# Kernel tuning notes

Hardware: AMD Instinct MI355X
Metric: run time of the kernel (lower is better)

The kernel has to match this reference:

```python
import jax, jax.numpy as jnp
import numpy as np

B, T, IDIM, ODIM, HDIM, CDIM = 8, 8192, 256, 256, 1024, 128


def setup_inputs() -> dict:
    key = jax.random.key(0)
    ks = jax.random.split(key, 7)
    s_enc = 1.0 / np.sqrt(IDIM)
    s_dec = 1.0 / np.sqrt(HDIM)
    return {
        "x": jax.random.normal(ks[0], (B, T, IDIM), jnp.float32),
        "mask_prev": jnp.zeros((B, T, HDIM), jnp.float32),
        "W_enc": jax.random.uniform(ks[1], (IDIM, HDIM), jnp.float32, -s_enc, s_enc),
        "b_enc": jax.random.uniform(ks[2], (HDIM,), jnp.float32, -s_enc, s_enc),
        "W_dec_self": jax.random.uniform(ks[3], (HDIM, IDIM), jnp.float32, -s_dec, s_dec),
        "b_dec_self": jax.random.uniform(ks[4], (IDIM,), jnp.float32, -s_dec, s_dec),
        "W_dec_src": jax.random.uniform(ks[5], (HDIM, ODIM), jnp.float32, -s_dec, s_dec),
        "b_dec_src": jax.random.uniform(ks[6], (ODIM,), jnp.float32, -s_dec, s_dec),
        "decoder_type": 0,  # 0 = 'self', 1 = 'src'
    }


def _topk_masks(h, cdim):
    # energy_pooling_mask with share=True: topk(k=2*cdim) of h^2 along hdim.
    energy = h * h  # [B,T,H]
    _, idx = jax.lax.top_k(energy, 2 * cdim)  # [B,T,2C] indices into H
    bi = jnp.arange(h.shape[0])[:, None, None]
    ti = jnp.arange(h.shape[1])[None, :, None]
    # scatter instead of materializing one_hot [B,T,2C,H]
    mask = jnp.zeros_like(h).at[bi, ti, idx[..., :cdim]].add(1.0)
    mask_share = jnp.zeros_like(h).at[bi, ti, idx].add(1.0)
    return mask, mask_share


def reference(x, mask_prev, W_enc, b_enc, W_dec_self, b_dec_self, W_dec_src, b_dec_src, decoder_type):
    # encoder
    h = jnp.einsum("bti,ih->bth", x, W_enc) + b_enc  # [B,T,H]
    # hidden_exclude_activation (mask_prev provided): zero previously-used units
    h = jnp.where(mask_prev > 0, 0.0, h)
    mask_cur, mask_cur_share = _topk_masks(h, CDIM)
    mask_new = mask_prev + mask_cur
    h = jnp.where(mask_cur_share > 0, h, 0.0)
    # decoder (idim == odim asserted in original)
    if decoder_type == 0:
        out = jnp.einsum("bth,ho->bto", h, W_dec_self) + b_dec_self
    else:
        out = jnp.einsum("bth,ho->bto", h, W_dec_src) + b_dec_src
    return out, mask_new
```

## Files before the change

kernel.cpp:

```cpp
#include <hip/hip_runtime.h>
#include <hip/hip_bf16.h>

#define B_ 8
#define T_ 8192
#define M_ (B_ * T_)
#define IDIM 256
#define HDIM 1024
#define ODIM 256
#define CDIM 128
#define OUT_OFF ((size_t)M_ * ODIM)

typedef __attribute__((ext_vector_type(4))) float floatx4;
typedef __attribute__((ext_vector_type(8))) short shortx8;

__global__ __launch_bounds__(256) void k0_convw(const float* __restrict__ Wself,
                                                const float* __restrict__ Wsrc,
                                                const int* __restrict__ dtype,
                                                __hip_bfloat16* __restrict__ WdT) {
    int id = blockIdx.x * 256 + threadIdx.x;
    int n = id >> 10;
    int k = id & 1023;
    const float* W = (*dtype == 0) ? Wself : Wsrc;
    WdT[id] = __float2bfloat16(W[(size_t)k * ODIM + n]);
}

__global__ __launch_bounds__(256) void k1_enc(const float* __restrict__ X,
                                              const float* __restrict__ W,
                                              const float* __restrict__ bias,
                                              float* __restrict__ H) {
    __shared__ __align__(16) float As[32][132];
    __shared__ __align__(16) float Bs[32][128];
    const int t  = threadIdx.x;
    const int m0 = blockIdx.x * 128;
    const int n0 = blockIdx.y * 128;
    const int tx = t & 15;
    const int ty = t >> 4;

    float acc[8][8];
#pragma unroll
    for (int i = 0; i < 8; ++i)
#pragma unroll
        for (int j = 0; j < 8; ++j) acc[i][j] = 0.0f;

    for (int kk = 0; kk < IDIM; kk += 32) {
#pragma unroll
        for (int r = 0; r < 4; ++r) {
            int idx = t + r * 256;
            int row = idx >> 3;
            int k4  = (idx & 7) << 2;
            float4 a = *(const float4*)(X + (size_t)(m0 + row) * IDIM + kk + k4);
            As[k4 + 0][row] = a.x;
            As[k4 + 1][row] = a.y;
            As[k4 + 2][row] = a.z;
            As[k4 + 3][row] = a.w;
        }
#pragma unroll
        for (int r = 0; r < 4; ++r) {
            int idx = t + r * 256;
            int row = idx >> 5;
            int c4  = (idx & 31) << 2;
            *(float4*)&Bs[row][c4] =
                *(const float4*)(W + (size_t)(kk + row) * HDIM + n0 + c4);
        }
        __syncthreads();

#pragma unroll 8
        for (int k = 0; k < 32; ++k) {
            float4 a0 = *(const float4*)&As[k][ty * 8];
            float4 a1 = *(const float4*)&As[k][ty * 8 + 4];
            float4 b0 = *(const float4*)&Bs[k][tx * 4];
            float4 b1 = *(const float4*)&Bs[k][tx * 4 + 64];
            float av[8] = {a0.x, a0.y, a0.z, a0.w, a1.x, a1.y, a1.z, a1.w};
            float bv[8] = {b0.x, b0.y, b0.z, b0.w, b1.x, b1.y, b1.z, b1.w};
#pragma unroll
            for (int i = 0; i < 8; ++i)
#pragma unroll
                for (int j = 0; j < 8; ++j)
                    acc[i][j] = fmaf(av[i], bv[j], acc[i][j]);
        }
        __syncthreads();
    }

#pragma unroll
    for (int i = 0; i < 8; ++i) {
        int gm = m0 + ty * 8 + i;
        float* o = H + (size_t)gm * HDIM + n0;
        float4 v0, v1;
        v0.x = acc[i][0] + bias[n0 + tx * 4 + 0];
        v0.y = acc[i][1] + bias[n0 + tx * 4 + 1];
        v0.z = acc[i][2] + bias[n0 + tx * 4 + 2];
        v0.w = acc[i][3] + bias[n0 + tx * 4 + 3];
        v1.x = acc[i][4] + bias[n0 + 64 + tx * 4 + 0];
        v1.y = acc[i][5] + bias[n0 + 64 + tx * 4 + 1];
        v1.z = acc[i][6] + bias[n0 + 64 + tx * 4 + 2];
        v1.w = acc[i][7] + bias[n0 + 64 + tx * 4 + 3];
        *(float4*)(o + tx * 4) = v0;
        *(float4*)(o + 64 + tx * 4) = v1;
    }
}

__device__ __forceinline__ unsigned int radix_kth(const unsigned int* u, int k,
                                                  unsigned int* hist,
                                                  unsigned int* res,
                                                  int lane, int* r_out) {
    unsigned int prefix = 0;
    int kk = k;
    for (int pass = 3; pass >= 0; --pass) {
        const int sh = pass * 8;
        hist[lane] = 0u; hist[lane + 64] = 0u;
        hist[lane + 128] = 0u; hist[lane + 192] = 0u;
        __syncthreads();
#pragma unroll
        for (int i = 0; i < 16; ++i) {
            bool matched = (pass == 3) || ((u[i] >> (sh + 8)) == (prefix >> (sh + 8)));
            if (matched) atomicAdd(&hist[(u[i] >> sh) & 0xFFu], 1u);
        }
        __syncthreads();
        unsigned int c0 = hist[lane * 4 + 0], c1 = hist[lane * 4 + 1];
        unsigned int c2 = hist[lane * 4 + 2], c3 = hist[lane * 4 + 3];
        unsigned int lt = c0 + c1 + c2 + c3;
        unsigned int s = lt;
#pragma unroll
        for (int off = 1; off < 64; off <<= 1) {
            unsigned int o = (unsigned int)__shfl_down((int)s, off, 64);
            if (lane + off < 64) s += o;
        }
        unsigned int gt_lanes = s - lt;
        unsigned int cs[4] = {c0, c1, c2, c3};
        unsigned int sf[4] = {c1 + c2 + c3, c2 + c3, c3, 0u};
#pragma unroll
        for (int q = 0; q < 4; ++q) {
            int gt = (int)(gt_lanes + sf[q]);
            int ge = gt + (int)cs[q];
            if (gt < kk && kk <= ge) {
                res[0] = (unsigned int)(lane * 4 + q);
                res[1] = (unsigned int)gt;
            }
        }
        __syncthreads();
        unsigned int b = res[0];
        kk -= (int)res[1];
        prefix |= (b << sh);
        __syncthreads();
    }
    *r_out = kk;
    return prefix;
}

__global__ __launch_bounds__(256) void k2_topk(const float* __restrict__ mask_prev,
                                               float* __restrict__ Hio,
                                               __hip_bfloat16* __restrict__ Abf) {
    __shared__ unsigned int hist[4][256];
    __shared__ unsigned int res[4][2];
    const int t = threadIdx.x;
    const int wave = t >> 6;
    const int lane = t & 63;
    const size_t row = (size_t)blockIdx.x * 4 + wave;
    const float* mp = mask_prev + row * HDIM;
    float* hrow = Hio + row * HDIM;

    float hv[16], mpv[16];
    unsigned int u[16];
#pragma unroll
    for (int i = 0; i < 16; ++i) {
        int j = lane + (i << 6);
        float m = mp[j];
        float h = hrow[j];
        h = (m > 0.0f) ? 0.0f : h;
        mpv[i] = m; hv[i] = h;
        float e = h * h;
        u[i] = __float_as_uint(e);
    }

    int r1, r2;
    unsigned int T1 = radix_kth(u, CDIM,     hist[wave], res[wave], lane, &r1);
    unsigned int T2 = radix_kth(u, 2 * CDIM, hist[wave], res[wave], lane, &r2);

    const unsigned long long below = (1ULL << lane) - 1ULL;
    int c1 = 0, c2 = 0;
#pragma unroll
    for (int i = 0; i < 16; ++i) {
        unsigned long long b1 = __ballot(u[i] == T1);
        unsigned long long b2 = __ballot(u[i] == T2);
        bool s1 = (u[i] > T1) || ((u[i] == T1) && (c1 + __popcll(b1 & below) < r1));
        bool s2 = (u[i] > T2) || ((u[i] == T2) && (c2 + __popcll(b2 & below) < r2));
        c1 += __popcll(b1);
        c2 += __popcll(b2);
        int j = lane + (i << 6);
        hrow[j] = mpv[i] + (s1 ? 1.0f : 0.0f);
        Abf[row * HDIM + j] = __float2bfloat16(s2 ? hv[i] : 0.0f);
    }
}

__global__ __launch_bounds__(256) void k3_dec(const __hip_bfloat16* __restrict__ A,
                                              const __hip_bfloat16* __restrict__ Bt,
                                              const float* __restrict__ bias_self,
                                              const float* __restrict__ bias_src,
                                              const int* __restrict__ dtype,
                                              float* __restrict__ Out) {
    __shared__ __align__(16) __hip_bfloat16 As[128 * 32];
    __shared__ __align__(16) __hip_bfloat16 Bs[128 * 32];
    const int t = threadIdx.x;
    const int lane = t & 63;
    const int wave = t >> 6;
    const int m0 = blockIdx.x * 128;
    const int n0 = blockIdx.y * 128;
    const int wr = wave >> 1;
    const int wc = wave & 1;
    const int quad = lane >> 4;
    const int rf = lane & 15;

    floatx4 acc[4][4];
    const floatx4 z = {0.0f, 0.0f, 0.0f, 0.0f};
#pragma unroll
    for (int i = 0; i < 4; ++i)
#pragma unroll
        for (int j = 0; j < 4; ++j) acc[i][j] = z;

    for (int kk = 0; kk < HDIM; kk += 32) {
#pragma unroll
        for (int p = 0; p < 2; ++p) {
            int l = p * 256 + t;
            int row = l >> 2;
            int kc = (l & 3) << 3;
            *(uint4*)&As[row * 32 + kc] =
                *(const uint4*)(A + (size_t)(m0 + row) * HDIM + kk + kc);
            *(uint4*)&Bs[row * 32 + kc] =
                *(const uint4*)(Bt + (size_t)(n0 + row) * HDIM + kk + kc);
        }
        __syncthreads();

        shortx8 af[4], bf[4];
#pragma unroll
        for (int i = 0; i < 4; ++i) {
            af[i] = *(const shortx8*)&As[(wr * 64 + i * 16 + rf) * 32 + quad * 8];
            bf[i] = *(const shortx8*)&Bs[(wc * 64 + i * 16 + rf) * 32 + quad * 8];
        }
#pragma unroll
        for (int mi = 0; mi < 4; ++mi)
#pragma unroll
            for (int nj = 0; nj < 4; ++nj)
                acc[mi][nj] = __builtin_amdgcn_mfma_f32_16x16x32_bf16(
                    af[mi], bf[nj], acc[mi][nj], 0, 0, 0);
        __syncthreads();
    }

    const float* bias = (*dtype == 0) ? bias_self : bias_src;
#pragma unroll
    for (int mi = 0; mi < 4; ++mi) {
#pragma unroll
        for (int nj = 0; nj < 4; ++nj) {
            int gn = n0 + wc * 64 + nj * 16 + rf;
            float bv = bias[gn];
            int gmb = m0 + wr * 64 + mi * 16 + quad * 4;
#pragma unroll
            for (int r2 = 0; r2 < 4; ++r2)
                Out[(size_t)(gmb + r2) * ODIM + gn] = acc[mi][nj][r2] + bv;
        }
    }
}

extern "C" void kernel_launch(void* const* d_in, const int* in_sizes, int n_in,
                              void* d_out, int out_size, void* d_ws, size_t ws_size,
                              hipStream_t stream) {
    const float* x          = (const float*)d_in[0];
    const float* mask_prev  = (const float*)d_in[1];
    const float* W_enc      = (const float*)d_in[2];
    const float* b_enc      = (const float*)d_in[3];
    const float* W_dec_self = (const float*)d_in[4];
    const float* b_dec_self = (const float*)d_in[5];
    const float* W_dec_src  = (const float*)d_in[6];
    const float* b_dec_src  = (const float*)d_in[7];
    const int*   dtype      = (const int*)d_in[8];

    float* out  = (float*)d_out;
    float* Hbuf = out + OUT_OFF;

    __hip_bfloat16* Abf = (__hip_bfloat16*)d_ws;
    __hip_bfloat16* WdT = (__hip_bfloat16*)((char*)d_ws + (size_t)M_ * HDIM * 2);

    k0_convw<<<dim3((ODIM * HDIM) / 256), 256, 0, stream>>>(W_dec_self, W_dec_src, dtype, WdT);
    k1_enc  <<<dim3(M_ / 128, HDIM / 128), 256, 0, stream>>>(x, W_enc, b_enc, Hbuf);
    k2_topk <<<dim3(M_ / 4), 256, 0, stream>>>(mask_prev, Hbuf, Abf);
    k3_dec  <<<dim3(M_ / 128, ODIM / 128), 256, 0, stream>>>(Abf, WdT, b_dec_self, b_dec_src, dtype, out);
}
```

Before: 1.170 ms.

## Prefetch GEMM tiles into registers, pad decoder LDS, replace radix top-k with binned selection

```diff
diff --git a/kernel.cpp b/kernel.cpp
--- a/kernel.cpp
+++ b/kernel.cpp
@@ -36,34 +36,48 @@
     const int tx = t & 15;
     const int ty = t >> 4;
 
+    int arow[4], ak4[4], brow[4], bc4[4];
+#pragma unroll
+    for (int r = 0; r < 4; ++r) {
+        int idx = t + r * 256;
+        arow[r] = idx >> 3;
+        ak4[r]  = (idx & 7) << 2;
+        brow[r] = idx >> 5;
+        bc4[r]  = (idx & 31) << 2;
+    }
+
     float acc[8][8];
 #pragma unroll
     for (int i = 0; i < 8; ++i)
 #pragma unroll
         for (int j = 0; j < 8; ++j) acc[i][j] = 0.0f;
 
-    for (int kk = 0; kk < IDIM; kk += 32) {
-#pragma unroll
-        for (int r = 0; r < 4; ++r) {
-            int idx = t + r * 256;
-            int row = idx >> 3;
-            int k4  = (idx & 7) << 2;
-            float4 a = *(const float4*)(X + (size_t)(m0 + row) * IDIM + kk + k4);
-            As[k4 + 0][row] = a.x;
-            As[k4 + 1][row] = a.y;
-            As[k4 + 2][row] = a.z;
-            As[k4 + 3][row] = a.w;
-        }
-#pragma unroll
-        for (int r = 0; r < 4; ++r) {
-            int idx = t + r * 256;
-            int row = idx >> 5;
-            int c4  = (idx & 31) << 2;
-            *(float4*)&Bs[row][c4] =
-                *(const float4*)(W + (size_t)(kk + row) * HDIM + n0 + c4);
-        }
-        __syncthreads();
-
+    float4 apre[4], bpre[4];
+#pragma unroll
+    for (int r = 0; r < 4; ++r) {
+        apre[r] = *(const float4*)(X + (size_t)(m0 + arow[r]) * IDIM + ak4[r]);
+        bpre[r] = *(const float4*)(W + (size_t)brow[r] * HDIM + n0 + bc4[r]);
+    }
+#pragma unroll
+    for (int r = 0; r < 4; ++r) {
+        As[ak4[r] + 0][arow[r]] = apre[r].x;
+        As[ak4[r] + 1][arow[r]] = apre[r].y;
+        As[ak4[r] + 2][arow[r]] = apre[r].z;
+        As[ak4[r] + 3][arow[r]] = apre[r].w;
+        *(float4*)&Bs[brow[r]][bc4[r]] = bpre[r];
+    }
+    __syncthreads();
+
+#pragma unroll 1
+    for (int kt = 0; kt < 8; ++kt) {
+        if (kt < 7) {
+            int kn = (kt + 1) * 32;
+#pragma unroll
+            for (int r = 0; r < 4; ++r) {
+                apre[r] = *(const float4*)(X + (size_t)(m0 + arow[r]) * IDIM + kn + ak4[r]);
+                bpre[r] = *(const float4*)(W + (size_t)(kn + brow[r]) * HDIM + n0 + bc4[r]);
+            }
+        }
 #pragma unroll 8
         for (int k = 0; k < 32; ++k) {
             float4 a0 = *(const float4*)&As[k][ty * 8];
@@ -79,6 +93,17 @@
                     acc[i][j] = fmaf(av[i], bv[j], acc[i][j]);
         }
         __syncthreads();
+        if (kt < 7) {
+#pragma unroll
+            for (int r = 0; r < 4; ++r) {
+                As[ak4[r] + 0][arow[r]] = apre[r].x;
+                As[ak4[r] + 1][arow[r]] = apre[r].y;
+                As[ak4[r] + 2][arow[r]] = apre[r].z;
+                As[ak4[r] + 3][arow[r]] = apre[r].w;
+                *(float4*)&Bs[brow[r]][bc4[r]] = bpre[r];
+            }
+            __syncthreads();
+        }
     }
 
 #pragma unroll
@@ -99,59 +124,47 @@
     }
 }
 
-__device__ __forceinline__ unsigned int radix_kth(const unsigned int* u, int k,
-                                                  unsigned int* hist,
-                                                  unsigned int* res,
-                                                  int lane, int* r_out) {
-    unsigned int prefix = 0;
-    int kk = k;
-    for (int pass = 3; pass >= 0; --pass) {
-        const int sh = pass * 8;
-        hist[lane] = 0u; hist[lane + 64] = 0u;
-        hist[lane + 128] = 0u; hist[lane + 192] = 0u;
-        __syncthreads();
-#pragma unroll
-        for (int i = 0; i < 16; ++i) {
-            bool matched = (pass == 3) || ((u[i] >> (sh + 8)) == (prefix >> (sh + 8)));
-            if (matched) atomicAdd(&hist[(u[i] >> sh) & 0xFFu], 1u);
-        }
-        __syncthreads();
-        unsigned int c0 = hist[lane * 4 + 0], c1 = hist[lane * 4 + 1];
-        unsigned int c2 = hist[lane * 4 + 2], c3 = hist[lane * 4 + 3];
-        unsigned int lt = c0 + c1 + c2 + c3;
-        unsigned int s = lt;
+#define NBIN 512
+#define KBASE 1600
+#define CAP 128
+
+__device__ __forceinline__ unsigned int bsearch_kth(const unsigned int* u, int k,
+                                                    int lane, int* r_out) {
+    unsigned long long lo = 0, hi = 0xFFFFFFFFull;
+    while (lo < hi) {
+        unsigned int mid = (unsigned int)((lo + hi + 1) >> 1);
+        int c = 0;
+#pragma unroll
+        for (int i = 0; i < 16; ++i) c += (u[i] >= mid) ? 1 : 0;
 #pragma unroll
         for (int off = 1; off < 64; off <<= 1) {
-            unsigned int o = (unsigned int)__shfl_down((int)s, off, 64);
-            if (lane + off < 64) s += o;
-        }
-        unsigned int gt_lanes = s - lt;
-        unsigned int cs[4] = {c0, c1, c2, c3};
-        unsigned int sf[4] = {c1 + c2 + c3, c2 + c3, c3, 0u};
-#pragma unroll
-        for (int q = 0; q < 4; ++q) {
-            int gt = (int)(gt_lanes + sf[q]);
-            int ge = gt + (int)cs[q];
-            if (gt < kk && kk <= ge) {
-                res[0] = (unsigned int)(lane * 4 + q);
-                res[1] = (unsigned int)gt;
-            }
-        }
-        __syncthreads();
-        unsigned int b = res[0];
-        kk -= (int)res[1];
-        prefix |= (b << sh);
-        __syncthreads();
-    }
-    *r_out = kk;
-    return prefix;
+            int o = __shfl_down(c, off, 64);
+            if (lane + off < 64) c += o;
+        }
+        c = __shfl(c, 0);
+        if (c >= k) lo = mid; else hi = (unsigned long long)mid - 1;
+    }
+    unsigned int T = (unsigned int)lo;
+    int g = 0;
+#pragma unroll
+    for (int i = 0; i < 16; ++i) g += (u[i] > T) ? 1 : 0;
+#pragma unroll
+    for (int off = 1; off < 64; off <<= 1) {
+        int o = __shfl_down(g, off, 64);
+        if (lane + off < 64) g += o;
+    }
+    g = __shfl(g, 0);
+    *r_out = k - g;
+    return T;
 }
 
 __global__ __launch_bounds__(256) void k2_topk(const float* __restrict__ mask_prev,
                                                float* __restrict__ Hio,
                                                __hip_bfloat16* __restrict__ Abf) {
-    __shared__ unsigned int hist[4][256];
-    __shared__ unsigned int res[4][2];
+    __shared__ unsigned int hist[4][NBIN];
+    __shared__ unsigned long long cand[4][2][CAP];
+    __shared__ unsigned int sres[4][8];
+    __shared__ unsigned int scnt[4][2];
     const int t = threadIdx.x;
     const int wave = t >> 6;
     const int lane = t & 63;
@@ -161,6 +174,7 @@
 
     float hv[16], mpv[16];
     unsigned int u[16];
+    int bin[16];
 #pragma unroll
     for (int i = 0; i < 16; ++i) {
         int j = lane + (i << 6);
@@ -170,36 +184,118 @@
         mpv[i] = m; hv[i] = h;
         float e = h * h;
         u[i] = __float_as_uint(e);
-    }
-
-    int r1, r2;
-    unsigned int T1 = radix_kth(u, CDIM,     hist[wave], res[wave], lane, &r1);
-    unsigned int T2 = radix_kth(u, 2 * CDIM, hist[wave], res[wave], lane, &r2);
+        int b = (int)(u[i] >> 19) - KBASE;
+        bin[i] = (b < 0) ? 0 : ((b > NBIN - 1) ? NBIN - 1 : b);
+    }
+
+#pragma unroll
+    for (int q = 0; q < 8; ++q) hist[wave][lane + (q << 6)] = 0u;
+    if (lane < 2) scnt[wave][lane] = 0u;
+    __syncthreads();
+#pragma unroll
+    for (int i = 0; i < 16; ++i) atomicAdd(&hist[wave][bin[i]], 1u);
+    __syncthreads();
+
+    {
+        unsigned int cj[8]; unsigned int lt = 0;
+#pragma unroll
+        for (int jj = 0; jj < 8; ++jj) { cj[jj] = hist[wave][lane * 8 + jj]; lt += cj[jj]; }
+        unsigned int s = lt;
+#pragma unroll
+        for (int off = 1; off < 64; off <<= 1) {
+            unsigned int o = (unsigned int)__shfl_down((int)s, off, 64);
+            if (lane + off < 64) s += o;
+        }
+        unsigned int run = s - lt;
+#pragma unroll
+        for (int jj = 7; jj >= 0; --jj) {
+            unsigned int gt = run, ge = run + cj[jj];
+            if (gt < CDIM && CDIM <= ge)         { sres[wave][0] = lane * 8 + jj; sres[wave][1] = CDIM - gt; }
+            if (gt < 2 * CDIM && 2 * CDIM <= ge) { sres[wave][2] = lane * 8 + jj; sres[wave][3] = 2 * CDIM - gt; }
+            run = ge;
+        }
+    }
+    __syncthreads();
+    const unsigned int b1 = sres[wave][0], kk1 = sres[wave][1];
+    const unsigned int b2 = sres[wave][2], kk2 = sres[wave][3];
+
+#pragma unroll
+    for (int i = 0; i < 16; ++i) {
+        int j = lane + (i << 6);
+        unsigned long long pk = ((unsigned long long)u[i] << 32) | (unsigned int)(1023 - j);
+        if ((unsigned int)bin[i] == b1) {
+            unsigned int p = atomicAdd(&scnt[wave][0], 1u);
+            if (p < CAP) cand[wave][0][p] = pk;
+        }
+        if (b2 != b1 && (unsigned int)bin[i] == b2) {
+            unsigned int p = atomicAdd(&scnt[wave][1], 1u);
+            if (p < CAP) cand[wave][1][p] = pk;
+        }
+    }
+    __syncthreads();
+    const unsigned int C1 = scnt[wave][0];
+    const unsigned int C2 = (b2 == b1) ? C1 : scnt[wave][1];
+    const unsigned long long* L2 = (b2 == b1) ? cand[wave][0] : cand[wave][1];
+
+    if (C1 <= CAP) {
+        for (unsigned int idx = lane; idx < C1; idx += 64) {
+            unsigned long long mine = cand[wave][0][idx];
+            unsigned int myu = (unsigned int)(mine >> 32);
+            unsigned int rank = 0, gtu = 0;
+            for (unsigned int c = 0; c < C1; ++c) {
+                unsigned long long o = cand[wave][0][c];
+                rank += (o > mine) ? 1u : 0u;
+                gtu  += ((unsigned int)(o >> 32) > myu) ? 1u : 0u;
+            }
+            if (rank == kk1 - 1) { sres[wave][4] = myu; sres[wave][5] = gtu; }
+        }
+    }
+    if (C2 <= CAP) {
+        for (unsigned int idx = lane; idx < C2; idx += 64) {
+            unsigned long long mine = L2[idx];
+            unsigned int myu = (unsigned int)(mine >> 32);
+            unsigned int rank = 0, gtu = 0;
+            for (unsigned int c = 0; c < C2; ++c) {
+                unsigned long long o = L2[c];
+                rank += (o > mine) ? 1u : 0u;
+                gtu  += ((unsigned int)(o >> 32) > myu) ? 1u : 0u;
+            }
+            if (rank == kk2 - 1) { sres[wave][6] = myu; sres[wave][7] = gtu; }
+        }
+    }
+    __syncthreads();
+
+    unsigned int T1, T2; int r1, r2;
+    if (C1 <= CAP) { T1 = sres[wave][4]; r1 = (int)(kk1 - sres[wave][5]); }
+    else           { T1 = bsearch_kth(u, CDIM, lane, &r1); }
+    if (C2 <= CAP) { T2 = sres[wave][6]; r2 = (int)(kk2 - sres[wave][7]); }
+    else           { T2 = bsearch_kth(u, 2 * CDIM, lane, &r2); }
 
     const unsigned long long below = (1ULL << lane) - 1ULL;
     int c1 = 0, c2 = 0;
 #pragma unroll
     for (int i = 0; i < 16; ++i) {
-        unsigned long long b1 = __ballot(u[i] == T1);
-        unsigned long long b2 = __ballot(u[i] == T2);
-        bool s1 = (u[i] > T1) || ((u[i] == T1) && (c1 + __popcll(b1 & below) < r1));
-        bool s2 = (u[i] > T2) || ((u[i] == T2) && (c2 + __popcll(b2 & below) < r2));
-        c1 += __popcll(b1);
-        c2 += __popcll(b2);
+        unsigned long long bb1 = __ballot(u[i] == T1);
+        unsigned long long bb2 = __ballot(u[i] == T2);
+        bool s1 = (u[i] > T1) || ((u[i] == T1) && (c1 + (int)__popcll(bb1 & below) < r1));
+        bool s2 = (u[i] > T2) || ((u[i] == T2) && (c2 + (int)__popcll(bb2 & below) < r2));
+        c1 += (int)__popcll(bb1);
+        c2 += (int)__popcll(bb2);
         int j = lane + (i << 6);
         hrow[j] = mpv[i] + (s1 ? 1.0f : 0.0f);
         Abf[row * HDIM + j] = __float2bfloat16(s2 ? hv[i] : 0.0f);
     }
 }
 
+#define K3LD 40
 __global__ __launch_bounds__(256) void k3_dec(const __hip_bfloat16* __restrict__ A,
                                               const __hip_bfloat16* __restrict__ Bt,
                                               const float* __restrict__ bias_self,
                                               const float* __restrict__ bias_src,
                                               const int* __restrict__ dtype,
                                               float* __restrict__ Out) {
-    __shared__ __align__(16) __hip_bfloat16 As[128 * 32];
-    __shared__ __align__(16) __hip_bfloat16 Bs[128 * 32];
+    __shared__ __align__(16) __hip_bfloat16 As[128 * K3LD];
+    __shared__ __align__(16) __hip_bfloat16 Bs[128 * K3LD];
     const int t = threadIdx.x;
     const int lane = t & 63;
     const int wave = t >> 6;
@@ -210,6 +306,14 @@
     const int quad = lane >> 4;
     const int rf = lane & 15;
 
+    int srow[2], skc[2];
+#pragma unroll
+    for (int p = 0; p < 2; ++p) {
+        int l = p * 256 + t;
+        srow[p] = l >> 2;
+        skc[p]  = (l & 3) << 3;
+    }
+
     floatx4 acc[4][4];
     const floatx4 z = {0.0f, 0.0f, 0.0f, 0.0f};
 #pragma unroll
@@ -217,24 +321,34 @@
 #pragma unroll
         for (int j = 0; j < 4; ++j) acc[i][j] = z;
 
-    for (int kk = 0; kk < HDIM; kk += 32) {
-#pragma unroll
-        for (int p = 0; p < 2; ++p) {
-            int l = p * 256 + t;
-            int row = l >> 2;
-            int kc = (l & 3) << 3;
-            *(uint4*)&As[row * 32 + kc] =
-                *(const uint4*)(A + (size_t)(m0 + row) * HDIM + kk + kc);
-            *(uint4*)&Bs[row * 32 + kc] =
-                *(const uint4*)(Bt + (size_t)(n0 + row) * HDIM + kk + kc);
-        }
-        __syncthreads();
-
+    uint4 apre[2], bpre[2];
+#pragma unroll
+    for (int p = 0; p < 2; ++p) {
+        apre[p] = *(const uint4*)(A  + (size_t)(m0 + srow[p]) * HDIM + skc[p]);
+        bpre[p] = *(const uint4*)(Bt + (size_t)(n0 + srow[p]) * HDIM + skc[p]);
+    }
+#pragma unroll
+    for (int p = 0; p < 2; ++p) {
+        *(uint4*)&As[srow[p] * K3LD + skc[p]] = apre[p];
+        *(uint4*)&Bs[srow[p] * K3LD + skc[p]] = bpre[p];
+    }
+    __syncthreads();
+
+#pragma unroll 1
+    for (int kt = 0; kt < HDIM / 32; ++kt) {
+        if (kt < HDIM / 32 - 1) {
+            int kn = (kt + 1) * 32;
+#pragma unroll
+            for (int p = 0; p < 2; ++p) {
+                apre[p] = *(const uint4*)(A  + (size_t)(m0 + srow[p]) * HDIM + kn + skc[p]);
+                bpre[p] = *(const uint4*)(Bt + (size_t)(n0 + srow[p]) * HDIM + kn + skc[p]);
+            }
+        }
         shortx8 af[4], bf[4];
 #pragma unroll
         for (int i = 0; i < 4; ++i) {
-            af[i] = *(const shortx8*)&As[(wr * 64 + i * 16 + rf) * 32 + quad * 8];
-            bf[i] = *(const shortx8*)&Bs[(wc * 64 + i * 16 + rf) * 32 + quad * 8];
+            af[i] = *(const shortx8*)&As[(wr * 64 + i * 16 + rf) * K3LD + quad * 8];
+            bf[i] = *(const shortx8*)&Bs[(wc * 64 + i * 16 + rf) * K3LD + quad * 8];
         }
 #pragma unroll
         for (int mi = 0; mi < 4; ++mi)
@@ -243,6 +357,14 @@
                 acc[mi][nj] = __builtin_amdgcn_mfma_f32_16x16x32_bf16(
                     af[mi], bf[nj], acc[mi][nj], 0, 0, 0);
         __syncthreads();
+        if (kt < HDIM / 32 - 1) {
+#pragma unroll
+            for (int p = 0; p < 2; ++p) {
+                *(uint4*)&As[srow[p] * K3LD + skc[p]] = apre[p];
+                *(uint4*)&Bs[srow[p] * K3LD + skc[p]] = bpre[p];
+            }
+            __syncthreads();
+        }
     }
 
     const float* bias = (*dtype == 0) ? bias_self : bias_src;
```

Result: no change. 1.187 ms (+1.4%).
